# Optimization experiments

Hardware: AMD Instinct MI355X
Metric: run time of the kernel (lower is better)

## Reference

```python
import jax, jax.numpy as jnp
import numpy as np


def _apply_rope(x, rope):
    # x: (B, T, D); rope: (T, D//2, 2) broadcast over batch
    B, T, D = x.shape
    x_ = x.reshape(B, T, D // 2, 2)
    cos, sin = rope[..., 0], rope[..., 1]
    xr, xi = x_[..., 0], x_[..., 1]
    rotr = xr * cos - xi * sin
    roti = xr * sin + xi * cos
    return jnp.stack([rotr, roti], axis=-1).reshape(B, T, D)


def setup_inputs() -> dict:
    key = jax.random.key(0)
    k1, k2, k3, k4 = jax.random.split(key, 4)
    B, T, D, H = 2, 2048, 1024, 16
    x = jax.random.normal(k1, (B, T, D), dtype=jnp.float32)
    rope = jax.random.normal(k2, (T, D // 2, 2), dtype=jnp.float32)
    w_qkv = jax.random.normal(k3, (3 * D, D), dtype=jnp.float32) * (1.0 / np.sqrt(D))
    w_proj = jax.random.normal(k4, (D, D), dtype=jnp.float32) * (1.0 / np.sqrt(D))
    return {"x": x, "rope": rope, "w_qkv": w_qkv, "w_proj": w_proj}


def reference(x, rope, w_qkv, w_proj):
    B, T, D = x.shape
    H = 16
    dk = D // H
    qkv = jnp.einsum("btd,ed->bte", x, w_qkv)  # (B, T, 3D)
    q, k, v = jnp.split(qkv, 3, axis=-1)
    q = _apply_rope(q, rope)
    k = _apply_rope(k, rope)
    # split heads: (B, H, T, dk)
    q = q.reshape(B, T, H, dk).transpose(0, 2, 1, 3)
    k = k.reshape(B, T, H, dk).transpose(0, 2, 1, 3)
    v = v.reshape(B, T, H, dk).transpose(0, 2, 1, 3)
    att = jnp.einsum("bhqd,bhkd->bhqk", q, k) / jnp.sqrt(jnp.float32(dk)).astype(x.dtype)
    att = jax.nn.softmax(att, axis=-1)
    out = jnp.einsum("bhqk,bhkd->bhqd", att, v)
    out = out.transpose(0, 2, 1, 3).reshape(B, T, D)
    return jnp.einsum("btd,ed->bte", out, w_proj)
```

## Files before the change

kernel.cpp:

```cpp
#include <hip/hip_runtime.h>

typedef _Float16 f16;
typedef _Float16 f16x2 __attribute__((ext_vector_type(2)));
typedef _Float16 f16x4 __attribute__((ext_vector_type(4)));
typedef _Float16 f16x8 __attribute__((ext_vector_type(8)));
typedef float    f32x2 __attribute__((ext_vector_type(2)));
typedef float    f32x4 __attribute__((ext_vector_type(4)));
typedef short    s16x4 __attribute__((ext_vector_type(4)));

#define GLDS16(gptr, lptr)                                                     \
  __builtin_amdgcn_global_load_lds(                                            \
      (const __attribute__((address_space(1))) void*)(gptr),                   \
      (__attribute__((address_space(3))) void*)(lptr), 16, 0, 0)

#define S_BARRIER() __builtin_amdgcn_s_barrier()
#define FENCE() asm volatile("" ::: "memory")
#define WAIT_VM4() asm volatile("s_waitcnt vmcnt(4)" ::: "memory")
#define WAIT_VM0() asm volatile("s_waitcnt vmcnt(0)" ::: "memory")
#define WAIT_LGKM0() asm volatile("s_waitcnt lgkmcnt(0)" ::: "memory")
#define SETPRIO(x) __builtin_amdgcn_s_setprio(x)

__device__ inline short f32_to_bf16_rne(float f) {
  unsigned u = __builtin_bit_cast(unsigned, f);
  return (short)((u + 0x7FFFu + ((u >> 16) & 1u)) >> 16);
}

__global__ __launch_bounds__(256) void k_cast3(const float* __restrict__ a,
                                               const float* __restrict__ b,
                                               const float* __restrict__ c,
                                               f16* __restrict__ oa,
                                               f16* __restrict__ ob,
                                               f16* __restrict__ oc) {
  int i = blockIdx.x * 256 + threadIdx.x;
  const float* src;
  f16* dst;
  int off;
  if (i < 1048576) { src = a; dst = oa; off = i; }
  else if (i < 1835008) { src = b; dst = ob; off = i - 1048576; }
  else { src = c; dst = oc; off = i - 1835008; }
  f32x4 v = ((const f32x4*)src)[off];
  f16x4 h;
  h[0] = (f16)v[0]; h[1] = (f16)v[1]; h[2] = (f16)v[2]; h[3] = (f16)v[3];
  ((f16x4*)dst)[off] = h;
}

__global__ __launch_bounds__(256, 4) void k_gemm_qkv(
    const f16* __restrict__ A, const f16* __restrict__ B,
    const float* __restrict__ rope, f16* __restrict__ qh,
    f16* __restrict__ kh, short* __restrict__ vt) {
  const int K = 1024;
  __shared__ f16 sA[128 * 64];
  __shared__ f16 sB[128 * 64];
  const int tid = threadIdx.x;
  const int wave = tid >> 6, lane = tid & 63;
  const int lr = lane & 15, lq = lane >> 4;
  const int lr7 = lr & 7;
  const int wm = (wave >> 1) * 64, wn = (wave & 1) * 64;
  const size_t m0 = (size_t)blockIdx.x * 128, n0 = (size_t)blockIdx.y * 128;

  f32x4 acc[4][4] = {};

  const int sw8 = ((tid & 7) ^ ((tid >> 3) & 7)) * 8;
  const f16* ga = A + (m0 + (tid >> 3)) * (size_t)K + sw8;
  const f16* gb = B + (n0 + (tid >> 3)) * (size_t)K + sw8;

  for (int k0 = 0; k0 < K; k0 += 64) {
    __syncthreads();
#pragma unroll
    for (int r = 0; r < 4; ++r) {
      GLDS16(ga + (size_t)(r * 32) * K + k0, (char*)sA + r * 4096 + wave * 1024);
      GLDS16(gb + (size_t)(r * 32) * K + k0, (char*)sB + r * 4096 + wave * 1024);
    }
    __syncthreads();

#pragma unroll
    for (int kk = 0; kk < 2; ++kk) {
      f16x8 af[4], bf[4];
#pragma unroll
      for (int i = 0; i < 4; ++i)
        af[i] = *(const f16x8*)&sA[(wm + i * 16 + lr) * 64 +
                                   (((kk * 4 + lq) ^ lr7) * 8)];
#pragma unroll
      for (int j = 0; j < 4; ++j)
        bf[j] = *(const f16x8*)&sB[(wn + j * 16 + lr) * 64 +
                                   (((kk * 4 + lq) ^ lr7) * 8)];
#pragma unroll
      for (int i = 0; i < 4; ++i)
#pragma unroll
        for (int j = 0; j < 4; ++j)
          acc[i][j] = __builtin_amdgcn_mfma_f32_16x16x32_f16(af[i], bf[j],
                                                             acc[i][j], 0, 0, 0);
    }
  }

  const int region = (int)(n0 >> 10);
  if (region == 2) {
#pragma unroll
    for (int i = 0; i < 4; ++i)
#pragma unroll
      for (int j = 0; j < 4; ++j) {
        int e = (int)(n0 + wn + j * 16 + lr) - 2048;
        int h = e >> 6, c = e & 63;
        int d = c >> 4, lrv = c & 15;
        int m = (int)(m0 + wm + i * 16 + lq * 4);
        int b = m >> 11, t0 = m & 2047;
        int jcc = t0 >> 7, kv = t0 & 127;
        int ks = kv >> 4, lqv = (kv >> 2) & 3;
        s16x4 o;
#pragma unroll
        for (int r = 0; r < 4; ++r) o[r] = f32_to_bf16_rne(acc[i][j][r]);
        size_t idx =
            ((((size_t)((b * 16 + h) * 16 + jcc)) * 32 + d * 8 + ks) * 64 +
             lqv * 16 + lrv) * 4;
        *(s16x4*)&vt[idx] = o;
      }
  } else {
    const float scl = region == 0 ? 0.1803368801111204f : 1.0f;
    f16* dst = region == 0 ? qh : kh;
    const int odd = lr & 1;
#pragma unroll
    for (int i = 0; i < 4; ++i)
#pragma unroll
      for (int j = 0; j < 4; ++j) {
        int e = ((int)(n0 + wn + j * 16 + lr)) & 1023;
        int h = e >> 6, c = e & 63, p = e >> 1;
        int mb = (int)(m0 + wm + i * 16 + lq * 4);
        int b = mb >> 11;
#pragma unroll
        for (int r = 0; r < 4; ++r) {
          int t = (mb + r) & 2047;
          float v = acc[i][j][r];
          float partner = __shfl_xor(v, 1);
          f32x2 cs = *(const f32x2*)&rope[((size_t)t * 512 + p) * 2];
          float out = odd ? (partner * cs[1] + v * cs[0])
                          : (v * cs[0] - partner * cs[1]);
          dst[(((size_t)(b * 16 + h)) * 2048 + t) * 64 + c] = (f16)(out * scl);
        }
      }
  }
}

__global__ __launch_bounds__(256, 2) void k_gemm_bt(const f16* __restrict__ A,
                                                    const f16* __restrict__ B,
                                                    float* __restrict__ C,
                                                    int M, int N, int K) {
  __shared__ f16 sA[2][128 * 64];
  __shared__ f16 sB[2][128 * 64];
  const int tid = threadIdx.x;
  const int wave = tid >> 6, lane = tid & 63;
  const int lr = lane & 15, lq = lane >> 4;
  const int lr7 = lr & 7;
  const int wm = (wave >> 1) * 64, wn = (wave & 1) * 64;
  const size_t m0 = (size_t)blockIdx.x * 128, n0 = (size_t)blockIdx.y * 128;

  f32x4 acc[4][4] = {};

  const int sw8 = ((tid & 7) ^ ((tid >> 3) & 7)) * 8;
  const f16* ga = A + (m0 + (tid >> 3)) * (size_t)K + sw8;
  const f16* gb = B + (n0 + (tid >> 3)) * (size_t)K + sw8;

  auto stage = [&](int k0, int d) {
#pragma unroll
    for (int r = 0; r < 4; ++r) {
      GLDS16(ga + (size_t)(r * 32) * K + k0,
             (char*)&sA[d][0] + r * 4096 + wave * 1024);
      GLDS16(gb + (size_t)(r * 32) * K + k0,
             (char*)&sB[d][0] + r * 4096 + wave * 1024);
    }
  };

  stage(0, 0);

  for (int k0 = 0; k0 < K; k0 += 64) {
    const int cur = (k0 >> 6) & 1;
    WAIT_VM0();
    WAIT_LGKM0();
    S_BARRIER();
    FENCE();
    if (k0 + 64 < K) stage(k0 + 64, cur ^ 1);

#pragma unroll
    for (int kk = 0; kk < 2; ++kk) {
      f16x8 af[4], bf[4];
#pragma unroll
      for (int i = 0; i < 4; ++i)
        af[i] = *(const f16x8*)&sA[cur][(wm + i * 16 + lr) * 64 +
                                       (((kk * 4 + lq) ^ lr7) * 8)];
#pragma unroll
      for (int j = 0; j < 4; ++j)
        bf[j] = *(const f16x8*)&sB[cur][(wn + j * 16 + lr) * 64 +
                                       (((kk * 4 + lq) ^ lr7) * 8)];
#pragma unroll
      for (int i = 0; i < 4; ++i)
#pragma unroll
        for (int j = 0; j < 4; ++j)
          acc[i][j] = __builtin_amdgcn_mfma_f32_16x16x32_f16(af[i], bf[j],
                                                             acc[i][j], 0, 0, 0);
    }
  }

#pragma unroll
  for (int i = 0; i < 4; ++i)
#pragma unroll
    for (int j = 0; j < 4; ++j)
#pragma unroll
      for (int r = 0; r < 4; ++r)
        C[(m0 + wm + i * 16 + lq * 4 + r) * (size_t)N + n0 + wn + j * 16 + lr] =
            acc[i][j][r];
}

__global__ __launch_bounds__(512, 4) void k_attn(const f16* __restrict__ Qp,
                                                 const f16* __restrict__ Kp,
                                                 const short* __restrict__ Vt,
                                                 f16* __restrict__ Op) {
  __shared__ f16 sQ[128 * 64];
  __shared__ f16 sKV[2 * 16384];
  const int tid = threadIdx.x, wave = tid >> 6, lane = tid & 63;
  const int lr = lane & 15, lq = lane >> 4;
  const int lr7 = lr & 7;
  const int qg = wave & 3, kg = wave >> 2;
  const int bh = blockIdx.x, qt = blockIdx.y;
  const size_t base = (size_t)bh * 2048 * 64;

  const int sw8 = ((tid & 7) ^ ((tid >> 3) & 7)) * 8;

  auto stage_kv = [&](int jcc, int d) {
    const f16* gk = Kp + base + (size_t)jcc * 128 * 64;
    const short* gv = Vt + (size_t)(bh * 16 + jcc) * 8192;
    char* bK = (char*)sKV + d * 32768;
    char* bV = bK + 16384;
#pragma unroll
    for (int r = 0; r < 2; ++r) {
      GLDS16(gk + (size_t)(r * 64 + (tid >> 3)) * 64 + sw8,
             bK + r * 8192 + wave * 1024);
      GLDS16(gv + (size_t)(r * 512 + tid) * 8,
             bV + r * 8192 + wave * 1024);
    }
  };

  const f16* gq = Qp + base + (size_t)qt * 128 * 64;
#pragma unroll
  for (int r = 0; r < 2; ++r)
    GLDS16(gq + (size_t)(r * 64 + (tid >> 3)) * 64 + sw8,
           (char*)sQ + r * 8192 + wave * 1024);
  stage_kv(0, 0);
  WAIT_VM4();
  S_BARRIER();
  FENCE();
  const int qrow = qg * 32 + lr;
  f16x8 qa0 = *(const f16x8*)&sQ[qrow * 64 + ((lq ^ lr7) * 8)];
  f16x8 qa1 = *(const f16x8*)&sQ[qrow * 64 + (((4 + lq) ^ lr7) * 8)];
  f16x8 qb0 = *(const f16x8*)&sQ[(qrow + 16) * 64 + ((lq ^ lr7) * 8)];
  f16x8 qb1 = *(const f16x8*)&sQ[(qrow + 16) * 64 + (((4 + lq) ^ lr7) * 8)];

  f32x4 ota[4] = {}, otb[4] = {};
  float la = 0.f, lb = 0.f;
  const int ntbase = kg * 4;

#pragma unroll 1
  for (int jc = 0; jc < 16; ++jc) {
    const int cur = jc & 1;
    WAIT_VM0();
    WAIT_LGKM0();
    S_BARRIER();
    FENCE();
    if (jc < 15) stage_kv(jc + 1, cur ^ 1);

    const f16* bK = (const f16*)((char*)sKV + cur * 32768);
    const short* bV = (const short*)((char*)sKV + cur * 32768 + 16384);

#pragma unroll
    for (int nt4 = 0; nt4 < 4; ++nt4) {
      const int nt = ntbase + nt4;
      f16x8 kf0 = *(const f16x8*)&bK[(nt * 16 + lr) * 64 + ((lq ^ lr7) * 8)];
      f16x8 kf1 =
          *(const f16x8*)&bK[(nt * 16 + lr) * 64 + (((4 + lq) ^ lr7) * 8)];
      f32x4 z = {0.f, 0.f, 0.f, 0.f};
      SETPRIO(1);
      f32x4 sa = __builtin_amdgcn_mfma_f32_16x16x32_f16(kf0, qa0, z, 0, 0, 0);
      sa = __builtin_amdgcn_mfma_f32_16x16x32_f16(kf1, qa1, sa, 0, 0, 0);
      f32x4 sb = __builtin_amdgcn_mfma_f32_16x16x32_f16(kf0, qb0, z, 0, 0, 0);
      sb = __builtin_amdgcn_mfma_f32_16x16x32_f16(kf1, qb1, sb, 0, 0, 0);
      SETPRIO(0);
      s16x4 pfa, pfb;
#pragma unroll
      for (int r = 0; r < 4; ++r) {
        float pa = __builtin_amdgcn_exp2f(sa[r]);
        float pb = __builtin_amdgcn_exp2f(sb[r]);
        la += pa; lb += pb;
        pfa[r] = (short)(__builtin_bit_cast(unsigned, pa) >> 16);
        pfb[r] = (short)(__builtin_bit_cast(unsigned, pb) >> 16);
      }
      SETPRIO(1);
#pragma unroll
      for (int d = 0; d < 4; ++d) {
        s16x4 vf = *(const s16x4*)&bV[((d * 8 + nt) * 64 + lane) * 4];
        ota[d] = __builtin_amdgcn_mfma_f32_16x16x16bf16_1k(vf, pfa, ota[d],
                                                           0, 0, 0);
        otb[d] = __builtin_amdgcn_mfma_f32_16x16x16bf16_1k(vf, pfb, otb[d],
                                                           0, 0, 0);
      }
      SETPRIO(0);
    }
  }

  la += __shfl_xor(la, 16); la += __shfl_xor(la, 32);
  lb += __shfl_xor(lb, 16); lb += __shfl_xor(lb, 32);

  float* os = (float*)((char*)sKV + qg * 8192);
  float* ls = (float*)sQ;
  if (kg) {
#pragma unroll
    for (int d = 0; d < 4; ++d) {
      *(f32x4*)&os[(d * 64 + lane) * 4] = ota[d];
      *(f32x4*)&os[((4 + d) * 64 + lane) * 4] = otb[d];
    }
    if (lq == 0) { ls[qg * 32 + lr] = la; ls[qg * 32 + 16 + lr] = lb; }
  }
  WAIT_LGKM0();
  S_BARRIER();
  FENCE();
  if (kg) return;

#pragma unroll
  for (int d = 0; d < 4; ++d) {
    f32x4 pa_ = *(const f32x4*)&os[(d * 64 + lane) * 4];
    f32x4 pb_ = *(const f32x4*)&os[((4 + d) * 64 + lane) * 4];
#pragma unroll
    for (int r = 0; r < 4; ++r) { ota[d][r] += pa_[r]; otb[d][r] += pb_[r]; }
  }
  la += ls[qg * 32 + lr];
  lb += ls[qg * 32 + 16 + lr];

  float rla = 1.f / la, rlb = 1.f / lb;
  int b = bh >> 4, h = bh & 15;
  int ta = qt * 128 + qg * 32 + lr;
  f16* gouta = Op + ((size_t)(b * 2048 + ta)) * 1024 + h * 64;
  f16* goutb = gouta + (size_t)16 * 1024;
#pragma unroll
  for (int d = 0; d < 4; ++d) {
    f16x4 oa, ob;
#pragma unroll
    for (int r = 0; r < 4; ++r) {
      oa[r] = (f16)(ota[d][r] * rla);
      ob[r] = (f16)(otb[d][r] * rlb);
    }
    *(f16x4*)&gouta[d * 16 + lq * 4] = oa;
    *(f16x4*)&goutb[d * 16 + lq * 4] = ob;
  }
}

extern "C" void kernel_launch(void* const* d_in, const int* in_sizes, int n_in,
                              void* d_out, int out_size, void* d_ws,
                              size_t ws_size, hipStream_t stream) {
  const float* x     = (const float*)d_in[0];
  const float* rope  = (const float*)d_in[1];
  const float* wqkv  = (const float*)d_in[2];
  const float* wproj = (const float*)d_in[3];
  float* out = (float*)d_out;

  char* w = (char*)d_ws;
  const size_t MB = 1024 * 1024;
  f16* xh   = (f16*)(w + 0);
  f16* wqh  = (f16*)(w + 8 * MB);
  f16* wph  = (f16*)(w + 14 * MB);
  f16* qh   = (f16*)(w + 16 * MB);
  f16* kh   = (f16*)(w + 24 * MB);
  short* vth = (short*)(w + 32 * MB);
  f16* aoh  = (f16*)(w + 40 * MB);

  k_cast3<<<8192, 256, 0, stream>>>(x, wqkv, wproj, xh, wqh, wph);

  k_gemm_qkv<<<dim3(32, 24), 256, 0, stream>>>(xh, wqh, rope, qh, kh, vth);

  k_attn<<<dim3(32, 16), 512, 0, stream>>>(qh, kh, vth, aoh);

  k_gemm_bt<<<dim3(32, 8), 256, 0, stream>>>(aoh, wph, out, 4096, 1024, 1024);
}
```

Measured before the change: 194.4 us.

## Use 16x16x32 bf16 MFMA for PV by pairing key tiles

The PV product now uses the K=32 bf16 MFMA instead of the K=16 variant, pairing two 16-key score tiles into one 8-element P fragment. To match, the V-transpose layout written by the QKV GEMM epilogue is changed to 8-element groups, and the K rows staged into LDS are permuted so that the paired score tiles line up with the key order of the V fragments. This halves the number of PV MFMA issues and uses wider LDS reads for V. The row permutation and the new V layout must agree exactly for results to stay correct.

```diff
diff --git a/kernel.cpp b/kernel.cpp
--- a/kernel.cpp
+++ b/kernel.cpp
@@ -7,6 +7,7 @@
 typedef float    f32x2 __attribute__((ext_vector_type(2)));
 typedef float    f32x4 __attribute__((ext_vector_type(4)));
 typedef short    s16x4 __attribute__((ext_vector_type(4)));
+typedef short    s16x8 __attribute__((ext_vector_type(8)));
 
 #define GLDS16(gptr, lptr)                                                     \
   __builtin_amdgcn_global_load_lds(                                            \
@@ -105,13 +106,15 @@
         int m = (int)(m0 + wm + i * 16 + lq * 4);
         int b = m >> 11, t0 = m & 2047;
         int jcc = t0 >> 7, kv = t0 & 127;
-        int ks = kv >> 4, lqv = (kv >> 2) & 3;
+        int mp = kv >> 5;
+        int lq8 = (kv >> 3) & 3;
+        int j0 = kv & 7;
         s16x4 o;
 #pragma unroll
         for (int r = 0; r < 4; ++r) o[r] = f32_to_bf16_rne(acc[i][j][r]);
         size_t idx =
-            ((((size_t)((b * 16 + h) * 16 + jcc)) * 32 + d * 8 + ks) * 64 +
-             lqv * 16 + lrv) * 4;
+            ((((size_t)((b * 16 + h) * 16 + jcc)) * 16 + d * 4 + mp) * 64 +
+             lq8 * 16 + lrv) * 8 + j0;
         *(s16x4*)&vt[idx] = o;
       }
   } else {
@@ -231,8 +234,10 @@
     char* bV = bK + 16384;
 #pragma unroll
     for (int r = 0; r < 2; ++r) {
-      GLDS16(gk + (size_t)(r * 64 + (tid >> 3)) * 64 + sw8,
-             bK + r * 8192 + wave * 1024);
+      int R = r * 64 + (tid >> 3);
+      int gRow = (R & ~31) |
+                 ((((R >> 2) & 3) << 3) | (((R >> 4) & 1) << 2) | (R & 3));
+      GLDS16(gk + (size_t)gRow * 64 + sw8, bK + r * 8192 + wave * 1024);
       GLDS16(gv + (size_t)(r * 512 + tid) * 8,
              bV + r * 8192 + wave * 1024);
     }
@@ -269,12 +274,13 @@
     const f16* bK = (const f16*)((char*)sKV + cur * 32768);
     const short* bV = (const short*)((char*)sKV + cur * 32768 + 16384);
 
-#pragma unroll
-    for (int nt4 = 0; nt4 < 4; ++nt4) {
-      const int nt = ntbase + nt4;
-      f16x8 kf0 = *(const f16x8*)&bK[(nt * 16 + lr) * 64 + ((lq ^ lr7) * 8)];
+    s16x4 plo_a, plo_b;
+#pragma unroll
+    for (int tt = 0; tt < 4; ++tt) {
+      const int t = ntbase + tt;
+      f16x8 kf0 = *(const f16x8*)&bK[(t * 16 + lr) * 64 + ((lq ^ lr7) * 8)];
       f16x8 kf1 =
-          *(const f16x8*)&bK[(nt * 16 + lr) * 64 + (((4 + lq) ^ lr7) * 8)];
+          *(const f16x8*)&bK[(t * 16 + lr) * 64 + (((4 + lq) ^ lr7) * 8)];
       f32x4 z = {0.f, 0.f, 0.f, 0.f};
       SETPRIO(1);
       f32x4 sa = __builtin_amdgcn_mfma_f32_16x16x32_f16(kf0, qa0, z, 0, 0, 0);
@@ -282,25 +288,34 @@
       f32x4 sb = __builtin_amdgcn_mfma_f32_16x16x32_f16(kf0, qb0, z, 0, 0, 0);
       sb = __builtin_amdgcn_mfma_f32_16x16x32_f16(kf1, qb1, sb, 0, 0, 0);
       SETPRIO(0);
-      s16x4 pfa, pfb;
+      s16x4 pa, pb;
 #pragma unroll
       for (int r = 0; r < 4; ++r) {
-        float pa = __builtin_amdgcn_exp2f(sa[r]);
-        float pb = __builtin_amdgcn_exp2f(sb[r]);
-        la += pa; lb += pb;
-        pfa[r] = (short)(__builtin_bit_cast(unsigned, pa) >> 16);
-        pfb[r] = (short)(__builtin_bit_cast(unsigned, pb) >> 16);
+        float va = __builtin_amdgcn_exp2f(sa[r]);
+        float vb = __builtin_amdgcn_exp2f(sb[r]);
+        la += va; lb += vb;
+        pa[r] = (short)(__builtin_bit_cast(unsigned, va) >> 16);
+        pb[r] = (short)(__builtin_bit_cast(unsigned, vb) >> 16);
       }
-      SETPRIO(1);
-#pragma unroll
-      for (int d = 0; d < 4; ++d) {
-        s16x4 vf = *(const s16x4*)&bV[((d * 8 + nt) * 64 + lane) * 4];
-        ota[d] = __builtin_amdgcn_mfma_f32_16x16x16bf16_1k(vf, pfa, ota[d],
+      if ((tt & 1) == 0) {
+        plo_a = pa; plo_b = pb;
+      } else {
+        s16x8 pa8 = {plo_a[0], plo_a[1], plo_a[2], plo_a[3],
+                     pa[0], pa[1], pa[2], pa[3]};
+        s16x8 pb8 = {plo_b[0], plo_b[1], plo_b[2], plo_b[3],
+                     pb[0], pb[1], pb[2], pb[3]};
+        const int mp = t >> 1;
+        SETPRIO(1);
+#pragma unroll
+        for (int d = 0; d < 4; ++d) {
+          s16x8 vf = *(const s16x8*)&bV[((d * 4 + mp) * 64 + lane) * 8];
+          ota[d] = __builtin_amdgcn_mfma_f32_16x16x32_bf16(vf, pa8, ota[d],
                                                            0, 0, 0);
-        otb[d] = __builtin_amdgcn_mfma_f32_16x16x16bf16_1k(vf, pfb, otb[d],
+          otb[d] = __builtin_amdgcn_mfma_f32_16x16x32_bf16(vf, pb8, otb[d],
                                                            0, 0, 0);
+        }
+        SETPRIO(0);
       }
-      SETPRIO(0);
     }
   }
 
```

After: 177.1 us. -8.9%, faster.
